# Performance work log

Measured on AMD Instinct MI355X. Metric: run time of the kernel, lower is better.

## Reference

```python
import jax, jax.numpy as jnp
import numpy as np

TOP_K = 2  # num_active_experts


def setup_inputs() -> dict:
    key = jax.random.key(0)
    k1, k2, k3 = jax.random.split(key, 3)
    N, D, E = 16384, 1024, 8
    x = jax.random.normal(k1, (N, D), dtype=jnp.float32)
    router_w = jax.random.normal(k2, (E, D), dtype=jnp.float32) * (1.0 / np.sqrt(D))
    router_b = jnp.zeros((E,), dtype=jnp.float32)
    expert_w = jax.random.normal(k3, (E, D, D), dtype=jnp.float32) * (1.0 / np.sqrt(D))
    expert_b = jnp.zeros((E, D), dtype=jnp.float32)
    return {"x": x, "router_w": router_w, "router_b": router_b,
            "expert_w": expert_w, "expert_b": expert_b}


def reference(x, router_w, router_b, expert_w, expert_b):
    E = router_w.shape[0]
    # Router: softmax over experts, pick top-k, renormalize
    logits = x @ router_w.T + router_b                      # [N, E]
    probs = jax.nn.softmax(logits, axis=-1)                 # [N, E]
    top_p, top_i = jax.lax.top_k(probs, TOP_K)              # [N, K]
    top_p = top_p / jnp.sum(top_p, axis=-1, keepdims=True)  # renormalized gates
    # Dense combine weights: [N, E], zero for non-selected experts
    combine = jnp.sum(jax.nn.one_hot(top_i, E, dtype=x.dtype) * top_p[..., None], axis=1)
    # All-expert outputs, then weighted combine (vectorized dispatch/combine)
    y = jnp.einsum('nd,eod->neo', x, expert_w) + expert_b   # [N, E, O]
    out = jnp.einsum('neo,ne->no', y, combine)              # [N, O]
    return out
```

## Files before the change

### kernel.cpp

```cpp
#include <hip/hip_runtime.h>
#include <hip/hip_bf16.h>


constexpr int DIMS = 1024;
constexpr int NE   = 8;
constexpr int ROUTER_BLOCKS = 1024;
constexpr int WCONV_BLOCKS  = NE * DIMS * DIMS / (8 * 256);
constexpr int BM = 192, BN = 256, BK = 64;
constexpr int RT_PER_XCD = 23;

typedef __attribute__((ext_vector_type(8))) short short8;
typedef __attribute__((ext_vector_type(4))) short short4_t;
typedef __attribute__((ext_vector_type(4))) float f32x4;

typedef const __attribute__((address_space(1))) void* gp_t;
typedef __attribute__((address_space(3))) void* sp_t;

__device__ __forceinline__ float b2f(unsigned short u) {
  union { unsigned int i; float f; } x; x.i = ((unsigned)u) << 16; return x.f;
}
__device__ __forceinline__ short f2bs(float f) {
  __hip_bfloat16 h = __float2bfloat16(f);
  return *(short*)&h;
}

__global__ __launch_bounds__(256) void prep_kernel(
    const float* __restrict__ x, const float* __restrict__ rw,
    const float* __restrict__ rb, const float* __restrict__ ew,
    __hip_bfloat16* __restrict__ xb, __hip_bfloat16* __restrict__ wb,
    int* __restrict__ blk_cnt, int* __restrict__ tmp_meta,
    float* __restrict__ tmp_gate, int n_tok) {
  const int tid = threadIdx.x;

  if ((int)blockIdx.x >= ROUTER_BLOCKS) {
    unsigned g = (unsigned)(blockIdx.x - ROUTER_BLOCKS) * 256 + tid;
    const float4* src = (const float4*)(ew + (size_t)g * 8);
    float4 a = src[0], b = src[1];
    union { __hip_bfloat16 h[8]; float4 f; } u;
    u.h[0] = __float2bfloat16(a.x); u.h[1] = __float2bfloat16(a.y);
    u.h[2] = __float2bfloat16(a.z); u.h[3] = __float2bfloat16(a.w);
    u.h[4] = __float2bfloat16(b.x); u.h[5] = __float2bfloat16(b.y);
    u.h[6] = __float2bfloat16(b.z); u.h[7] = __float2bfloat16(b.w);
    ((float4*)wb)[g] = u.f;
    return;
  }

  __shared__ float s_rw[NE * DIMS];
  __shared__ int s_cnt[NE];
  __shared__ int s_e[32];
  __shared__ float s_g[32];
  __shared__ int s_pos[32];

  const float4* rw4g = (const float4*)rw;
  float4* s4 = (float4*)s_rw;
  for (int i = tid; i < NE * DIMS / 4; i += 256) s4[i] = rw4g[i];
  if (tid < NE) s_cnt[tid] = 0;
  __syncthreads();

  const float4* s_rw4 = (const float4*)s_rw;
  const int wave = tid >> 6, lane = tid & 63;
  for (int i = 0; i < 4; ++i) {
    int t = blockIdx.x * 16 + wave * 4 + i;
    const float4* xr = (const float4*)(x + (size_t)t * DIMS);
    short4_t* xw = (short4_t*)(xb + (size_t)t * DIMS);
    float a[NE];
#pragma unroll
    for (int e = 0; e < NE; ++e) a[e] = 0.f;
#pragma unroll
    for (int j = 0; j < 4; ++j) {
      float4 v = xr[lane + j * 64];
      short4_t p;
      p[0] = f2bs(v.x); p[1] = f2bs(v.y); p[2] = f2bs(v.z); p[3] = f2bs(v.w);
      xw[lane + j * 64] = p;
#pragma unroll
      for (int e = 0; e < NE; ++e) {
        float4 w = s_rw4[e * 256 + lane + j * 64];
        a[e] = fmaf(v.x, w.x, fmaf(v.y, w.y, fmaf(v.z, w.z, fmaf(v.w, w.w, a[e]))));
      }
    }
#pragma unroll
    for (int off = 32; off > 0; off >>= 1) {
#pragma unroll
      for (int e = 0; e < NE; ++e) a[e] += __shfl_xor(a[e], off, 64);
    }
    if (lane == 0) {
      float l[NE];
#pragma unroll
      for (int e = 0; e < NE; ++e) l[e] = a[e] + rb[e];
      int e0 = 0;
#pragma unroll
      for (int e = 1; e < NE; ++e) if (l[e] > l[e0]) e0 = e;
      int e1 = (e0 == 0) ? 1 : 0;
#pragma unroll
      for (int e = 0; e < NE; ++e) if (e != e0 && l[e] > l[e1]) e1 = e;
      float r = expf(l[e1] - l[e0]);
      float g0 = 1.f / (1.f + r);
      float g1 = 1.f - g0;
      int ai = (wave * 4 + i) * 2;
      int p0 = atomicAdd(&s_cnt[e0], 1);
      int p1 = atomicAdd(&s_cnt[e1], 1);
      s_e[ai] = e0; s_g[ai] = g0; s_pos[ai] = p0;
      s_e[ai + 1] = e1; s_g[ai + 1] = g1; s_pos[ai + 1] = p1;
    }
  }
  __syncthreads();
  if (tid < NE) blk_cnt[blockIdx.x * NE + tid] = s_cnt[tid];
  if (tid < 32) {
    int s = blockIdx.x * 32 + tid;
    tmp_meta[s] = s_e[tid] | (s_pos[tid] << 3);
    tmp_gate[s] = s_g[tid];
  }
}

__global__ __launch_bounds__(512) void scan_kernel(
    const int* __restrict__ blk_cnt, int* __restrict__ blk_base,
    int* __restrict__ counts) {
  const int e = threadIdx.x >> 6, lane = threadIdx.x & 63;
  int running = 0;
  for (int c = 0; c < ROUTER_BLOCKS / 64; ++c) {
    int v = blk_cnt[(c * 64 + lane) * NE + e];
    int incl = v;
#pragma unroll
    for (int off = 1; off < 64; off <<= 1) {
      int t = __shfl_up(incl, off, 64);
      if (lane >= off) incl += t;
    }
    blk_base[(c * 64 + lane) * NE + e] = running + incl - v;
    running += __shfl(incl, 63, 64);
  }
  if (lane == 0) counts[e] = running;
}

__global__ __launch_bounds__(256) void scatter_kernel(
    const int* __restrict__ tmp_meta, const float* __restrict__ tmp_gate,
    const int* __restrict__ blk_base, int* __restrict__ entries,
    float* __restrict__ gates, int n_tok) {
  int s = blockIdx.x * 256 + threadIdx.x;
  int meta = tmp_meta[s];
  int e = meta & 7, pos = meta >> 3;
  int p = blk_base[(s >> 5) * NE + e] + pos;
  entries[e * n_tok + p] = ((s >> 1) << 1) | (s & 1);
  gates[e * n_tok + p] = tmp_gate[s];
}

__global__ __launch_bounds__(512, 2) void moe_gemm(
    const __hip_bfloat16* __restrict__ xb, const __hip_bfloat16* __restrict__ wb,
    const float* __restrict__ eb, const int* __restrict__ counts,
    const int* __restrict__ entries, const float* __restrict__ gates,
    __hip_bfloat16* __restrict__ y, int n_tok) {
  const int xcd = blockIdx.x & 7;
  const int j = blockIdx.x >> 3;
  const int ct = j & 3;
  const int virt = xcd * RT_PER_XCD + (j >> 2);

  int e = -1, rt = 0, cnt = 0, acc_t = 0;
#pragma unroll
  for (int i = 0; i < NE; ++i) {
    int c = counts[i];
    int t = (c + BM - 1) / BM;
    if (e < 0 && virt < acc_t + t) { e = i; rt = virt - acc_t; cnt = c; }
    acc_t += t;
  }
  if (e < 0) return;

  __shared__ __align__(16) char smem[2 * 24576 + 2 * 32768];

  const int tid = threadIdx.x;
  const int l = tid & 63, w = tid >> 6;
  const int row0 = rt * BM;
  const int n0 = ct * BN;

  const int qsw = (l & 7) ^ (l >> 3);
  const __hip_bfloat16* aptr[3];
  const __hip_bfloat16* bptr[4];
#pragma unroll
  for (int i = 0; i < 3; ++i) {
    int R = (i * 8 + w) * 8 + (l >> 3);
    int gr = row0 + R;
    int ent = (gr < cnt) ? entries[e * n_tok + gr] : 0;
    aptr[i] = xb + (size_t)(ent >> 1) * DIMS + qsw * 8;
  }
#pragma unroll
  for (int i = 0; i < 4; ++i) {
    int R = (i * 8 + w) * 8 + (l >> 3);
    bptr[i] = wb + ((size_t)e << 20) + (size_t)(n0 + R) * DIMS + qsw * 8;
  }

  const int fr = l & 15, quad = l >> 4;
  const int wr = w >> 2, wc = w & 3;
  const int swz = (quad ^ (fr & 7)) << 4;
  const int aoff0 = (wr * 96 + fr) * 128 + swz;
  const int boff0 = (wc * 64 + fr) * 128 + swz;

  auto stage = [&](int buf, int kt) {
    const int koff = kt * 64;
#pragma unroll
    for (int i = 0; i < 3; ++i)
      __builtin_amdgcn_global_load_lds(
          (gp_t)(aptr[i] + koff),
          (sp_t)(smem + buf * 24576 + (i * 8 + w) * 1024 + l * 16), 16, 0, 0);
#pragma unroll
    for (int i = 0; i < 4; ++i)
      __builtin_amdgcn_global_load_lds(
          (gp_t)(bptr[i] + koff),
          (sp_t)(smem + 49152 + buf * 32768 + (i * 8 + w) * 1024 + l * 16), 16, 0, 0);
  };

  f32x4 acc[6][4] = {};

  stage(0, 0);
  stage(1, 1);
  asm volatile("s_waitcnt vmcnt(7)" ::: "memory");
  __builtin_amdgcn_s_barrier();

  auto body = [&](int kt, int mode) {
    const int cur = kt & 1;
    const char* As = smem + cur * 24576;
    const char* Bs = smem + 49152 + cur * 32768;
    short8 af[6], bf[4];
#pragma unroll
    for (int mt = 0; mt < 6; ++mt) af[mt] = *(const short8*)(As + aoff0 + mt * 2048);
#pragma unroll
    for (int nt = 0; nt < 4; ++nt) bf[nt] = *(const short8*)(Bs + boff0 + nt * 2048);
    __builtin_amdgcn_s_setprio(1);
#pragma unroll
    for (int mt = 0; mt < 6; ++mt)
#pragma unroll
      for (int nt = 0; nt < 4; ++nt)
        acc[mt][nt] = __builtin_amdgcn_mfma_f32_16x16x32_bf16(af[mt], bf[nt], acc[mt][nt], 0, 0, 0);
    __builtin_amdgcn_s_setprio(0);
    short8 af2[6], bf2[4];
#pragma unroll
    for (int mt = 0; mt < 6; ++mt) af2[mt] = *(const short8*)(As + ((aoff0 + mt * 2048) ^ 64));
#pragma unroll
    for (int nt = 0; nt < 4; ++nt) bf2[nt] = *(const short8*)(Bs + ((boff0 + nt * 2048) ^ 64));
    asm volatile("s_waitcnt lgkmcnt(0)" ::: "memory");
    __builtin_amdgcn_s_barrier();
    if (mode == 0) stage(cur, kt + 2);
    __builtin_amdgcn_s_setprio(1);
#pragma unroll
    for (int mt = 0; mt < 6; ++mt)
#pragma unroll
      for (int nt = 0; nt < 4; ++nt)
        acc[mt][nt] = __builtin_amdgcn_mfma_f32_16x16x32_bf16(af2[mt], bf2[nt], acc[mt][nt], 0, 0, 0);
    __builtin_amdgcn_s_setprio(0);
    if (mode == 0) {
      asm volatile("s_waitcnt vmcnt(7)" ::: "memory");
      __builtin_amdgcn_s_barrier();
    } else if (mode == 1) {
      asm volatile("s_waitcnt vmcnt(0)" ::: "memory");
      __builtin_amdgcn_s_barrier();
    }
  };

#pragma unroll 1
  for (int kt = 0; kt < 14; ++kt) body(kt, 0);
  body(14, 1);
  body(15, 2);

  float bias[4];
#pragma unroll
  for (int nt = 0; nt < 4; ++nt) bias[nt] = eb[e * DIMS + n0 + wc * 64 + nt * 16 + fr];
#pragma unroll
  for (int mt = 0; mt < 6; ++mt) {
#pragma unroll
    for (int r = 0; r < 4; ++r) {
      int m = wr * 96 + mt * 16 + quad * 4 + r;
      int gr = row0 + m;
      if (gr < cnt) {
        int ent = entries[e * n_tok + gr];
        float g = gates[e * n_tok + gr];
        __hip_bfloat16* yp = y + (size_t)ent * DIMS + n0 + wc * 64 + fr;
#pragma unroll
        for (int nt = 0; nt < 4; ++nt)
          yp[nt * 16] = __float2bfloat16(g * (acc[mt][nt][r] + bias[nt]));
      }
    }
  }
}

__global__ __launch_bounds__(256) void combine_kernel(const __hip_bfloat16* __restrict__ y,
                                                      float* __restrict__ out) {
  size_t idx = (size_t)blockIdx.x * 256 + threadIdx.x;
  size_t n = idx >> 7;
  int c = (int)(idx & 127) << 3;
  short8 v0 = *(const short8*)(y + (n * 2) * DIMS + c);
  short8 v1 = *(const short8*)(y + (n * 2 + 1) * DIMS + c);
  float4 o0, o1;
  o0.x = b2f((unsigned short)v0[0]) + b2f((unsigned short)v1[0]);
  o0.y = b2f((unsigned short)v0[1]) + b2f((unsigned short)v1[1]);
  o0.z = b2f((unsigned short)v0[2]) + b2f((unsigned short)v1[2]);
  o0.w = b2f((unsigned short)v0[3]) + b2f((unsigned short)v1[3]);
  o1.x = b2f((unsigned short)v0[4]) + b2f((unsigned short)v1[4]);
  o1.y = b2f((unsigned short)v0[5]) + b2f((unsigned short)v1[5]);
  o1.z = b2f((unsigned short)v0[6]) + b2f((unsigned short)v1[6]);
  o1.w = b2f((unsigned short)v0[7]) + b2f((unsigned short)v1[7]);
  float* op = out + n * DIMS + c;
  ((float4*)op)[0] = o0;
  ((float4*)op)[1] = o1;
}

extern "C" void kernel_launch(void* const* d_in, const int* in_sizes, int n_in,
                              void* d_out, int out_size, void* d_ws, size_t ws_size,
                              hipStream_t stream) {
  const float* x  = (const float*)d_in[0];
  const float* rw = (const float*)d_in[1];
  const float* rb = (const float*)d_in[2];
  const float* ew = (const float*)d_in[3];
  const float* eb = (const float*)d_in[4];
  float* out = (float*)d_out;
  const int n_tok = in_sizes[0] / DIMS;
  const int n_slot = 2 * n_tok;

  char* ws = (char*)d_ws;
  size_t off = 0;
  int* counts = (int*)ws;                      off += 256;
  int* blk_cnt = (int*)(ws + off);             off += (size_t)ROUTER_BLOCKS * NE * 4;
  int* blk_base = (int*)(ws + off);            off += (size_t)ROUTER_BLOCKS * NE * 4;
  int* tmp_meta = (int*)(ws + off);            off += (size_t)n_slot * 4;
  float* tmp_gate = (float*)(ws + off);        off += (size_t)n_slot * 4;
  __hip_bfloat16* xb = (__hip_bfloat16*)(ws + off); off += (size_t)n_tok * DIMS * 2;
  __hip_bfloat16* wb = (__hip_bfloat16*)(ws + off); off += (size_t)NE * DIMS * DIMS * 2;
  int*   entries = (int*)(ws + off);           off += (size_t)NE * n_tok * 4;
  float* gates   = (float*)(ws + off);         off += (size_t)NE * n_tok * 4;
  __hip_bfloat16* y = (__hip_bfloat16*)(ws + off); off += (size_t)n_slot * DIMS * 2;
  if (ws_size < off) return;

  prep_kernel<<<ROUTER_BLOCKS + WCONV_BLOCKS, 256, 0, stream>>>(
      x, rw, rb, ew, xb, wb, blk_cnt, tmp_meta, tmp_gate, n_tok);
  scan_kernel<<<1, 512, 0, stream>>>(blk_cnt, blk_base, counts);
  scatter_kernel<<<n_slot / 256, 256, 0, stream>>>(
      tmp_meta, tmp_gate, blk_base, entries, gates, n_tok);
  moe_gemm<<<8 * RT_PER_XCD * 4, 512, 0, stream>>>(
      xb, wb, eb, counts, entries, gates, y, n_tok);
  combine_kernel<<<(unsigned)((size_t)n_tok * DIMS / 8 / 256), 256, 0, stream>>>(y, out);
}
```

Baseline: 266.4 us.

## Replace direct global-to-LDS loads with register-staged double buffering

Drops the global_load_lds async copies in the expert GEMM. Each k-tile is now loaded into registers one iteration ahead, written to the LDS double buffer, and followed by a single barrier per iteration. This simplifies the pipeline and removes the vmcnt-based staging modes. The cost is extra VGPR pressure and an explicit LDS write step, and global load latency is now hidden by only one tile of MFMA work instead of two.

Result: slower. 330.6 us (+24.1%).

```diff
diff --git a/kernel.cpp b/kernel.cpp
--- a/kernel.cpp
+++ b/kernel.cpp
@@ -12,9 +12,6 @@
 typedef __attribute__((ext_vector_type(8))) short short8;
 typedef __attribute__((ext_vector_type(4))) short short4_t;
 typedef __attribute__((ext_vector_type(4))) float f32x4;
-
-typedef const __attribute__((address_space(1))) void* gp_t;
-typedef __attribute__((address_space(3))) void* sp_t;
 
 __device__ __forceinline__ float b2f(unsigned short u) {
   union { unsigned int i; float f; } x; x.i = ((unsigned)u) << 16; return x.f;
@@ -170,7 +167,7 @@
   const int row0 = rt * BM;
   const int n0 = ct * BN;
 
-  const int qsw = (l & 7) ^ (l >> 3);
+  const int qsw = (l & 7) ^ ((l >> 3) & 7);
   const __hip_bfloat16* aptr[3];
   const __hip_bfloat16* bptr[4];
 #pragma unroll
@@ -186,37 +183,49 @@
     bptr[i] = wb + ((size_t)e << 20) + (size_t)(n0 + R) * DIMS + qsw * 8;
   }
 
+  char* awr[3];
+  char* bwr[4];
+#pragma unroll
+  for (int i = 0; i < 3; ++i) awr[i] = smem + (i * 8 + w) * 1024 + l * 16;
+#pragma unroll
+  for (int i = 0; i < 4; ++i) bwr[i] = smem + 49152 + (i * 8 + w) * 1024 + l * 16;
+
   const int fr = l & 15, quad = l >> 4;
   const int wr = w >> 2, wc = w & 3;
   const int swz = (quad ^ (fr & 7)) << 4;
   const int aoff0 = (wr * 96 + fr) * 128 + swz;
   const int boff0 = (wc * 64 + fr) * 128 + swz;
 
-  auto stage = [&](int buf, int kt) {
-    const int koff = kt * 64;
-#pragma unroll
-    for (int i = 0; i < 3; ++i)
-      __builtin_amdgcn_global_load_lds(
-          (gp_t)(aptr[i] + koff),
-          (sp_t)(smem + buf * 24576 + (i * 8 + w) * 1024 + l * 16), 16, 0, 0);
-#pragma unroll
-    for (int i = 0; i < 4; ++i)
-      __builtin_amdgcn_global_load_lds(
-          (gp_t)(bptr[i] + koff),
-          (sp_t)(smem + 49152 + buf * 32768 + (i * 8 + w) * 1024 + l * 16), 16, 0, 0);
-  };
-
   f32x4 acc[6][4] = {};
-
-  stage(0, 0);
-  stage(1, 1);
-  asm volatile("s_waitcnt vmcnt(7)" ::: "memory");
-  __builtin_amdgcn_s_barrier();
-
-  auto body = [&](int kt, int mode) {
+  float4 ra[3], rb4[4];
+
+#pragma unroll
+  for (int i = 0; i < 3; ++i) ra[i] = *(const float4*)(aptr[i]);
+#pragma unroll
+  for (int i = 0; i < 4; ++i) rb4[i] = *(const float4*)(bptr[i]);
+
+#pragma unroll 1
+  for (int kt = 0; kt < 16; ++kt) {
     const int cur = kt & 1;
-    const char* As = smem + cur * 24576;
-    const char* Bs = smem + 49152 + cur * 32768;
+    const int bufo = cur * 24576;
+    const int bufb = cur * 32768;
+#pragma unroll
+    for (int i = 0; i < 3; ++i) *(float4*)(awr[i] + bufo) = ra[i];
+#pragma unroll
+    for (int i = 0; i < 4; ++i) *(float4*)(bwr[i] + bufb) = rb4[i];
+    if (kt < 15) {
+      const int koff = (kt + 1) * 64;
+#pragma unroll
+      for (int i = 0; i < 3; ++i) ra[i] = *(const float4*)(aptr[i] + koff);
+#pragma unroll
+      for (int i = 0; i < 4; ++i) rb4[i] = *(const float4*)(bptr[i] + koff);
+    }
+    asm volatile("s_waitcnt lgkmcnt(0)" ::: "memory");
+    __builtin_amdgcn_s_barrier();
+    __builtin_amdgcn_sched_barrier(0);
+
+    const char* As = smem + bufo;
+    const char* Bs = smem + 49152 + bufb;
     short8 af[6], bf[4];
 #pragma unroll
     for (int mt = 0; mt < 6; ++mt) af[mt] = *(const short8*)(As + aoff0 + mt * 2048);
@@ -234,9 +243,6 @@
     for (int mt = 0; mt < 6; ++mt) af2[mt] = *(const short8*)(As + ((aoff0 + mt * 2048) ^ 64));
 #pragma unroll
     for (int nt = 0; nt < 4; ++nt) bf2[nt] = *(const short8*)(Bs + ((boff0 + nt * 2048) ^ 64));
-    asm volatile("s_waitcnt lgkmcnt(0)" ::: "memory");
-    __builtin_amdgcn_s_barrier();
-    if (mode == 0) stage(cur, kt + 2);
     __builtin_amdgcn_s_setprio(1);
 #pragma unroll
     for (int mt = 0; mt < 6; ++mt)
@@ -244,19 +250,7 @@
       for (int nt = 0; nt < 4; ++nt)
         acc[mt][nt] = __builtin_amdgcn_mfma_f32_16x16x32_bf16(af2[mt], bf2[nt], acc[mt][nt], 0, 0, 0);
     __builtin_amdgcn_s_setprio(0);
-    if (mode == 0) {
-      asm volatile("s_waitcnt vmcnt(7)" ::: "memory");
-      __builtin_amdgcn_s_barrier();
-    } else if (mode == 1) {
-      asm volatile("s_waitcnt vmcnt(0)" ::: "memory");
-      __builtin_amdgcn_s_barrier();
-    }
-  };
-
-#pragma unroll 1
-  for (int kt = 0; kt < 14; ++kt) body(kt, 0);
-  body(14, 1);
-  body(15, 2);
+  }
 
   float bias[4];
 #pragma unroll
```

## Retile MoE GEMM to 256x128 with split A/B staged half-step pipeline

Applied to the files above, without the earlier changes.

Changes the grouped expert GEMM tile from 192x256 to 256x128, with eight waves in a 4x2 layout each computing 64x64, and doubles the column-tile count in the grid. The K loop now issues B loads for the next step and A loads for two steps ahead separately. Each step's MFMA work is split into two halves separated by barriers, so more load traffic overlaps with compute. In exchange, each block does fewer flops per byte staged, adds more barriers, and uses 96KB of LDS.

Measured after the change: 292.2 us. 1.1x slower.

```diff
diff --git a/kernel.cpp b/kernel.cpp
--- a/kernel.cpp
+++ b/kernel.cpp
@@ -6,8 +6,8 @@
 constexpr int NE   = 8;
 constexpr int ROUTER_BLOCKS = 1024;
 constexpr int WCONV_BLOCKS  = NE * DIMS * DIMS / (8 * 256);
-constexpr int BM = 192, BN = 256, BK = 64;
-constexpr int RT_PER_XCD = 23;
+constexpr int BM = 256, BN = 128, BK = 64;
+constexpr int RT_PER_XCD = 17;
 
 typedef __attribute__((ext_vector_type(8))) short short8;
 typedef __attribute__((ext_vector_type(4))) short short4_t;
@@ -150,8 +150,8 @@
     __hip_bfloat16* __restrict__ y, int n_tok) {
   const int xcd = blockIdx.x & 7;
   const int j = blockIdx.x >> 3;
-  const int ct = j & 3;
-  const int virt = xcd * RT_PER_XCD + (j >> 2);
+  const int ct = j & 7;
+  const int virt = xcd * RT_PER_XCD + (j >> 3);
 
   int e = -1, rt = 0, cnt = 0, acc_t = 0;
 #pragma unroll
@@ -163,7 +163,7 @@
   }
   if (e < 0) return;
 
-  __shared__ __align__(16) char smem[2 * 24576 + 2 * 32768];
+  __shared__ __align__(16) char smem[98304];
 
   const int tid = threadIdx.x;
   const int l = tid & 63, w = tid >> 6;
@@ -171,101 +171,115 @@
   const int n0 = ct * BN;
 
   const int qsw = (l & 7) ^ (l >> 3);
-  const __hip_bfloat16* aptr[3];
-  const __hip_bfloat16* bptr[4];
-#pragma unroll
-  for (int i = 0; i < 3; ++i) {
-    int R = (i * 8 + w) * 8 + (l >> 3);
+  const __hip_bfloat16* aptr[4];
+  const __hip_bfloat16* bptr[2];
+#pragma unroll
+  for (int i = 0; i < 4; ++i) {
+    int R = (tid >> 3) + i * 64;
     int gr = row0 + R;
     int ent = (gr < cnt) ? entries[e * n_tok + gr] : 0;
     aptr[i] = xb + (size_t)(ent >> 1) * DIMS + qsw * 8;
   }
 #pragma unroll
-  for (int i = 0; i < 4; ++i) {
-    int R = (i * 8 + w) * 8 + (l >> 3);
+  for (int i = 0; i < 2; ++i) {
+    int R = (tid >> 3) + i * 64;
     bptr[i] = wb + ((size_t)e << 20) + (size_t)(n0 + R) * DIMS + qsw * 8;
   }
 
   const int fr = l & 15, quad = l >> 4;
-  const int wr = w >> 2, wc = w & 3;
+  const int wr = w >> 1, wc = w & 1;
   const int swz = (quad ^ (fr & 7)) << 4;
-  const int aoff0 = (wr * 96 + fr) * 128 + swz;
+  const int aoff0 = (wr * 64 + fr) * 128 + swz;
   const int boff0 = (wc * 64 + fr) * 128 + swz;
 
-  auto stage = [&](int buf, int kt) {
+  auto stageA = [&](int buf, int kt) {
     const int koff = kt * 64;
 #pragma unroll
-    for (int i = 0; i < 3; ++i)
+    for (int i = 0; i < 4; ++i)
       __builtin_amdgcn_global_load_lds(
           (gp_t)(aptr[i] + koff),
-          (sp_t)(smem + buf * 24576 + (i * 8 + w) * 1024 + l * 16), 16, 0, 0);
-#pragma unroll
-    for (int i = 0; i < 4; ++i)
+          (sp_t)(smem + buf * 32768 + tid * 16 + i * 8192), 16, 0, 0);
+  };
+  auto stageB = [&](int buf, int kt) {
+    const int koff = kt * 64;
+#pragma unroll
+    for (int i = 0; i < 2; ++i)
       __builtin_amdgcn_global_load_lds(
           (gp_t)(bptr[i] + koff),
-          (sp_t)(smem + 49152 + buf * 32768 + (i * 8 + w) * 1024 + l * 16), 16, 0, 0);
+          (sp_t)(smem + 65536 + buf * 16384 + tid * 16 + i * 8192), 16, 0, 0);
   };
 
-  f32x4 acc[6][4] = {};
-
-  stage(0, 0);
-  stage(1, 1);
-  asm volatile("s_waitcnt vmcnt(7)" ::: "memory");
+  f32x4 acc[4][4] = {};
+
+  stageA(0, 0);
+  stageB(0, 0);
+  stageA(1, 1);
+  asm volatile("s_waitcnt vmcnt(4)" ::: "memory");
   __builtin_amdgcn_s_barrier();
 
-  auto body = [&](int kt, int mode) {
-    const int cur = kt & 1;
-    const char* As = smem + cur * 24576;
-    const char* Bs = smem + 49152 + cur * 32768;
-    short8 af[6], bf[4];
-#pragma unroll
-    for (int mt = 0; mt < 6; ++mt) af[mt] = *(const short8*)(As + aoff0 + mt * 2048);
-#pragma unroll
-    for (int nt = 0; nt < 4; ++nt) bf[nt] = *(const short8*)(Bs + boff0 + nt * 2048);
+#pragma unroll 1
+  for (int t = 0; t < 16; ++t) {
+    const int cur = t & 1;
+    const char* As = smem + cur * 32768;
+    const char* Bs = smem + 65536 + cur * 16384;
+    short8 af[4][2], bf[4][2];
+
+#pragma unroll
+    for (int mt = 0; mt < 4; ++mt) {
+      af[mt][0] = *(const short8*)(As + aoff0 + mt * 2048);
+      af[mt][1] = *(const short8*)(As + ((aoff0 + mt * 2048) ^ 64));
+    }
+#pragma unroll
+    for (int nt = 0; nt < 2; ++nt) {
+      bf[nt][0] = *(const short8*)(Bs + boff0 + nt * 2048);
+      bf[nt][1] = *(const short8*)(Bs + ((boff0 + nt * 2048) ^ 64));
+    }
+    if (t + 1 < 16) stageB(cur ^ 1, t + 1);
+    __builtin_amdgcn_s_barrier();
+    asm volatile("s_waitcnt lgkmcnt(0)" ::: "memory");
+    __builtin_amdgcn_sched_barrier(0);
     __builtin_amdgcn_s_setprio(1);
 #pragma unroll
-    for (int mt = 0; mt < 6; ++mt)
-#pragma unroll
-      for (int nt = 0; nt < 4; ++nt)
-        acc[mt][nt] = __builtin_amdgcn_mfma_f32_16x16x32_bf16(af[mt], bf[nt], acc[mt][nt], 0, 0, 0);
+    for (int mt = 0; mt < 4; ++mt)
+#pragma unroll
+      for (int nt = 0; nt < 2; ++nt) {
+        acc[mt][nt] = __builtin_amdgcn_mfma_f32_16x16x32_bf16(af[mt][0], bf[nt][0], acc[mt][nt], 0, 0, 0);
+        acc[mt][nt] = __builtin_amdgcn_mfma_f32_16x16x32_bf16(af[mt][1], bf[nt][1], acc[mt][nt], 0, 0, 0);
+      }
     __builtin_amdgcn_s_setprio(0);
-    short8 af2[6], bf2[4];
-#pragma unroll
-    for (int mt = 0; mt < 6; ++mt) af2[mt] = *(const short8*)(As + ((aoff0 + mt * 2048) ^ 64));
-#pragma unroll
-    for (int nt = 0; nt < 4; ++nt) bf2[nt] = *(const short8*)(Bs + ((boff0 + nt * 2048) ^ 64));
+    __builtin_amdgcn_s_barrier();
+
+#pragma unroll
+    for (int nt = 2; nt < 4; ++nt) {
+      bf[nt][0] = *(const short8*)(Bs + boff0 + nt * 2048);
+      bf[nt][1] = *(const short8*)(Bs + ((boff0 + nt * 2048) ^ 64));
+    }
+    if (t + 2 < 16) stageA(cur, t + 2);
+    __builtin_amdgcn_s_barrier();
     asm volatile("s_waitcnt lgkmcnt(0)" ::: "memory");
+    __builtin_amdgcn_sched_barrier(0);
+    __builtin_amdgcn_s_setprio(1);
+#pragma unroll
+    for (int mt = 0; mt < 4; ++mt)
+#pragma unroll
+      for (int nt = 2; nt < 4; ++nt) {
+        acc[mt][nt] = __builtin_amdgcn_mfma_f32_16x16x32_bf16(af[mt][0], bf[nt][0], acc[mt][nt], 0, 0, 0);
+        acc[mt][nt] = __builtin_amdgcn_mfma_f32_16x16x32_bf16(af[mt][1], bf[nt][1], acc[mt][nt], 0, 0, 0);
+      }
+    __builtin_amdgcn_s_setprio(0);
+    if (t <= 13)      asm volatile("s_waitcnt vmcnt(4)" ::: "memory");
+    else if (t == 14) asm volatile("s_waitcnt vmcnt(0)" ::: "memory");
     __builtin_amdgcn_s_barrier();
-    if (mode == 0) stage(cur, kt + 2);
-    __builtin_amdgcn_s_setprio(1);
-#pragma unroll
-    for (int mt = 0; mt < 6; ++mt)
-#pragma unroll
-      for (int nt = 0; nt < 4; ++nt)
-        acc[mt][nt] = __builtin_amdgcn_mfma_f32_16x16x32_bf16(af2[mt], bf2[nt], acc[mt][nt], 0, 0, 0);
-    __builtin_amdgcn_s_setprio(0);
-    if (mode == 0) {
-      asm volatile("s_waitcnt vmcnt(7)" ::: "memory");
-      __builtin_amdgcn_s_barrier();
-    } else if (mode == 1) {
-      asm volatile("s_waitcnt vmcnt(0)" ::: "memory");
-      __builtin_amdgcn_s_barrier();
-    }
-  };
-
-#pragma unroll 1
-  for (int kt = 0; kt < 14; ++kt) body(kt, 0);
-  body(14, 1);
-  body(15, 2);
+  }
 
   float bias[4];
 #pragma unroll
   for (int nt = 0; nt < 4; ++nt) bias[nt] = eb[e * DIMS + n0 + wc * 64 + nt * 16 + fr];
 #pragma unroll
-  for (int mt = 0; mt < 6; ++mt) {
+  for (int mt = 0; mt < 4; ++mt) {
 #pragma unroll
     for (int r = 0; r < 4; ++r) {
-      int m = wr * 96 + mt * 16 + quad * 4 + r;
+      int m = wr * 64 + mt * 16 + quad * 4 + r;
       int gr = row0 + m;
       if (gr < cnt) {
         int ent = entries[e * n_tok + gr];
@@ -331,7 +345,7 @@
   scan_kernel<<<1, 512, 0, stream>>>(blk_cnt, blk_base, counts);
   scatter_kernel<<<n_slot / 256, 256, 0, stream>>>(
       tmp_meta, tmp_gate, blk_base, entries, gates, n_tok);
-  moe_gemm<<<8 * RT_PER_XCD * 4, 512, 0, stream>>>(
+  moe_gemm<<<8 * RT_PER_XCD * 8, 512, 0, stream>>>(
       xb, wb, eb, counts, entries, gates, y, n_tok);
   combine_kernel<<<(unsigned)((size_t)n_tok * DIMS / 8 / 256), 256, 0, stream>>>(y, out);
 }
```
